# Kernel optimization log

Measured on AMD Instinct MI355X. Metric: run time of the kernel, lower is better.

Reference implementation:

```python
import jax, jax.numpy as jnp
import numpy as np

C = 512
GROUPS = 32
EPS = 1e-6


def setup_inputs() -> dict:
    key = jax.random.key(0)
    ks = jax.random.split(key, 10)
    B, H, W = 4, 64, 64
    s = 0.02
    return {
        "x": jax.random.normal(ks[0], (B, C, H, W), dtype=jnp.float32),
        "gamma": jnp.ones((C,), jnp.float32),
        "beta": jnp.zeros((C,), jnp.float32),
        "Wq": jax.random.normal(ks[1], (C, C), jnp.float32) * s,
        "bq": jnp.zeros((C,), jnp.float32),
        "Wk": jax.random.normal(ks[2], (C, C), jnp.float32) * s,
        "bk": jnp.zeros((C,), jnp.float32),
        "Wv": jax.random.normal(ks[3], (C, C), jnp.float32) * s,
        "bv": jnp.zeros((C,), jnp.float32),
        "Wo": jax.random.normal(ks[4], (C, C), jnp.float32) * s,
        "bo": jnp.zeros((C,), jnp.float32),
    }


def _group_norm(x, gamma, beta):
    B, Cc, H, W = x.shape
    xg = x.reshape(B, GROUPS, Cc // GROUPS, H, W)
    mean = jnp.mean(xg, axis=(2, 3, 4), keepdims=True)
    var = jnp.var(xg, axis=(2, 3, 4), keepdims=True)
    xn = ((xg - mean) * jax.lax.rsqrt(var + EPS)).reshape(B, Cc, H, W)
    return xn * gamma[None, :, None, None] + beta[None, :, None, None]


def _conv1x1(x, Wm, b):
    # x: [B,C,H,W], Wm: [Cout,Cin]
    return jnp.einsum('bchw,oc->bohw', x, Wm) + b[None, :, None, None]


def reference(x, gamma, beta, Wq, bq, Wk, bk, Wv, bv, Wo, bo):
    B, Cc, H, W = x.shape
    h = _group_norm(x, gamma, beta)
    q = _conv1x1(h, Wq, bq).reshape(B, Cc, H * W)  # [B,C,N]
    k = _conv1x1(h, Wk, bk).reshape(B, Cc, H * W)
    v = _conv1x1(h, Wv, bv).reshape(B, Cc, H * W)
    scale = float(Cc) ** (-0.5)
    # attn[b,i,j] = sum_c q[b,c,i] k[b,c,j]
    attn = jnp.einsum('bci,bcj->bij', q, k) * scale
    attn = jax.nn.softmax(attn, axis=2)
    # out[b,c,i] = sum_j v[b,c,j] attn[b,i,j]
    out = jnp.einsum('bcj,bij->bci', v, attn).reshape(B, Cc, H, W)
    out = _conv1x1(out, Wo, bo)
    return x + out
```

## Files before the change

kernel.cpp:

```cpp
#include <hip/hip_runtime.h>
#include <hip/hip_bf16.h>


#define C_DIM 512
#define N_SPA 4096
#define BATCH 4
#define NALL 16384

#define BM 128
#define BN 128
#define BK 32

typedef short short8 __attribute__((ext_vector_type(8)));
typedef short short4v __attribute__((ext_vector_type(4)));
typedef float float4v __attribute__((ext_vector_type(4)));

__device__ __forceinline__ short f2b(float f) {
  __hip_bfloat16 h = __float2bfloat16(f);
  return *reinterpret_cast<short*>(&h);
}
__device__ __forceinline__ float b2f(short s) {
  __hip_bfloat16 h;
  *reinterpret_cast<short*>(&h) = s;
  return __bfloat162float(h);
}

typedef __attribute__((address_space(1))) const void gvoid_t;
typedef __attribute__((address_space(3))) void lvoid_t;
__device__ __forceinline__ void gload16(const void* g, void* l) {
  __builtin_amdgcn_global_load_lds((gvoid_t*)g, (lvoid_t*)l, 16, 0, 0);
}

__global__ void wconv_kernel(const float* __restrict__ Wq, const float* __restrict__ Wk,
                             const float* __restrict__ Wv, const float* __restrict__ Wo,
                             const float* __restrict__ bq, const float* __restrict__ bk,
                             const float* __restrict__ bv,
                             short* __restrict__ out, float* __restrict__ bias_all) {
  int i = blockIdx.x * 256 + threadIdx.x;
  out[0 * 262144 + i] = f2b(Wq[i]);
  out[1 * 262144 + i] = f2b(Wk[i]);
  out[2 * 262144 + i] = f2b(Wv[i]);
  out[3 * 262144 + i] = f2b(Wo[i]);
  if (i < 1536) bias_all[i] = (i < 512) ? bq[i] : (i < 1024) ? bk[i - 512] : bv[i - 1024];
}

__global__ void gn_part(const float* __restrict__ x, float2* __restrict__ partials) {
  int grp = blockIdx.x >> 5, split = blockIdx.x & 31;
  const float4* xg = (const float4*)(x + (size_t)grp * 65536 + split * 2048);
  int t = threadIdx.x;
  float4 a = xg[t], b4 = xg[256 + t];
  float s = a.x + a.y + a.z + a.w + b4.x + b4.y + b4.z + b4.w;
  float ss = a.x * a.x + a.y * a.y + a.z * a.z + a.w * a.w +
             b4.x * b4.x + b4.y * b4.y + b4.z * b4.z + b4.w * b4.w;
  __shared__ float red[512];
  red[t] = s; red[256 + t] = ss;
  __syncthreads();
  for (int off = 128; off > 0; off >>= 1) {
    if (t < off) { red[t] += red[t + off]; red[256 + t] += red[256 + t + off]; }
    __syncthreads();
  }
  if (t == 0) partials[blockIdx.x] = make_float2(red[0], red[256]);
}

__global__ void gn_norm(const float* __restrict__ x, const float* __restrict__ gamma,
                        const float* __restrict__ beta, const float2* __restrict__ partials,
                        short* __restrict__ h_t) {
  int bid = blockIdx.x;
  int grp = bid >> 4, seg = bid & 15;
  int b = grp >> 5, g = grp & 31;
  float s = 0.f, ss = 0.f;
  for (int j = 0; j < 32; ++j) { float2 p2 = partials[grp * 32 + j]; s += p2.x; ss += p2.y; }
  float mean = s * (1.0f / 65536.0f);
  float rstd = rsqrtf(ss * (1.0f / 65536.0f) - mean * mean + 1e-6f);

  const float* xg = x + (size_t)grp * 65536 + seg * 256;
  __shared__ float tile[16][257];
  int t = threadIdx.x;
#pragma unroll
  for (int i = 0; i < 16; ++i) tile[i][t] = xg[(size_t)i * N_SPA + t];
  __syncthreads();

  int c8 = (t & 1) * 8, ci = g * 16 + c8;
  float ga[8], be[8];
#pragma unroll
  for (int j = 0; j < 8; ++j) { ga[j] = gamma[ci + j]; be[j] = beta[ci + j]; }
#pragma unroll
  for (int pass = 0; pass < 2; ++pass) {
    int nl = (t >> 1) + pass * 128;
    short8 o;
#pragma unroll
    for (int j = 0; j < 8; ++j) {
      float v = (tile[c8 + j][nl] - mean) * rstd * ga[j] + be[j];
      o[j] = f2b(v);
    }
    *(short8*)&h_t[((size_t)b * N_SPA + seg * 256 + nl) * C_DIM + ci] = o;
  }
}

template <int EPI>
__global__ __launch_bounds__(256) void gemm_bt(
    const short* __restrict__ A, const short* __restrict__ BT, void* __restrict__ Cout,
    const float* __restrict__ bias, const float* __restrict__ resid,
    int M, int N, int K, int lda, int ldb, int ldc,
    size_t az, size_t bz, size_t cz, float scale) {
  __shared__ __align__(16) short lds_a[BM * BK];
  __shared__ __align__(16) short lds_b[BN * BK];
  int t = threadIdx.x;
  int m0 = blockIdx.y * BM;
  int n0 = blockIdx.x * BN;
  int z = blockIdx.z;
  A += (size_t)z * az;
  BT += (size_t)z * bz;
  int w = t >> 6, l = t & 63;
  int wm = (w >> 1) * 64, wn = (w & 1) * 64;
  int lr = l & 15, lk = l >> 4;

  int sr = l >> 2, scol = (l & 3) * 8;
  const short* ga0 = A + (size_t)(m0 + w * 16 + sr) * lda + scol;
  const short* ga1 = ga0 + (size_t)64 * lda;
  const short* gb0 = BT + (size_t)(n0 + w * 16 + sr) * ldb + scol;
  const short* gb1 = gb0 + (size_t)64 * ldb;
  short* la0 = &lds_a[w * 16 * BK];
  short* la1 = &lds_a[(64 + w * 16) * BK];
  short* lb0 = &lds_b[w * 16 * BK];
  short* lb1 = &lds_b[(64 + w * 16) * BK];

  float4v acc[4][4];
#pragma unroll
  for (int i = 0; i < 4; ++i)
#pragma unroll
    for (int j = 0; j < 4; ++j) acc[i][j] = (float4v){0.f, 0.f, 0.f, 0.f};

  for (int k0 = 0; k0 < K; k0 += BK) {
    __syncthreads();
    gload16(ga0, la0); gload16(ga1, la1);
    gload16(gb0, lb0); gload16(gb1, lb1);
    ga0 += BK; ga1 += BK; gb0 += BK; gb1 += BK;
    __syncthreads();
    short8 af[4], bf[4];
#pragma unroll
    for (int i = 0; i < 4; ++i) af[i] = *(const short8*)&lds_a[(wm + i * 16 + lr) * BK + lk * 8];
#pragma unroll
    for (int i = 0; i < 4; ++i) bf[i] = *(const short8*)&lds_b[(wn + i * 16 + lr) * BK + lk * 8];
#pragma unroll
    for (int i = 0; i < 4; ++i)
#pragma unroll
      for (int j = 0; j < 4; ++j)
        acc[i][j] = __builtin_amdgcn_mfma_f32_16x16x32_bf16(af[i], bf[j], acc[i][j], 0, 0, 0);
  }

#pragma unroll
  for (int i = 0; i < 4; ++i)
#pragma unroll
    for (int j = 0; j < 4; ++j) {
      int mB = m0 + wm + i * 16 + lk * 4;
      int nn = n0 + wn + j * 16 + lr;
      if constexpr (EPI == 2) {
        short* outp = (short*)Cout + (size_t)z * cz;
#pragma unroll
        for (int r = 0; r < 4; ++r)
          outp[(size_t)(mB + r) * ldc + nn] = f2b(__expf(acc[i][j][r] * scale));
      } else if constexpr (EPI == 3) {
        short* outp = (short*)Cout + (size_t)z * cz;
        float inv = bias[(size_t)z * N_SPA + nn];
        short4v v;
#pragma unroll
        for (int r = 0; r < 4; ++r) v[r] = f2b(acc[i][j][r] * inv);
        *(short4v*)(outp + (size_t)nn * ldc + mB) = v;
      } else if constexpr (EPI == 4) {
        int bb = nn >> 12, n = nn & 4095;
        size_t base = ((size_t)bb * C_DIM + mB) * N_SPA + n;
#pragma unroll
        for (int r = 0; r < 4; ++r) {
          float f = acc[i][j][r] + bias[mB + r] + resid[base + (size_t)r * N_SPA];
          ((float*)Cout)[base + (size_t)r * N_SPA] = f;
        }
      } else {
        short* outp = (short*)Cout + (size_t)z * NALL * C_DIM;
        const float* bz_ = bias + (size_t)z * C_DIM;
        if (z < 2) {
          short4v v;
#pragma unroll
          for (int r = 0; r < 4; ++r) v[r] = f2b(acc[i][j][r] + bz_[mB + r]);
          *(short4v*)(outp + (size_t)nn * C_DIM + mB) = v;
        } else {
#pragma unroll
          for (int r = 0; r < 4; ++r)
            outp[(size_t)(mB + r) * NALL + nn] = f2b(acc[i][j][r] + bz_[mB + r]);
        }
      }
    }
}

__global__ void rowsum_kernel(const short* __restrict__ p, float* __restrict__ inv_sum) {
  size_t row = blockIdx.x;
  const short8* pr = (const short8*)(p + row * N_SPA);
  int t = threadIdx.x;
  short8 a = pr[t * 2], b = pr[t * 2 + 1];
  float s = 0.f;
#pragma unroll
  for (int j = 0; j < 8; ++j) s += b2f(a[j]) + b2f(b[j]);
  __shared__ float red[256];
  red[t] = s; __syncthreads();
  for (int off = 128; off > 0; off >>= 1) {
    if (t < off) red[t] += red[t + off];
    __syncthreads();
  }
  if (t == 0) inv_sum[row] = 1.0f / red[0];
}

extern "C" void kernel_launch(void* const* d_in, const int* in_sizes, int n_in,
                              void* d_out, int out_size, void* d_ws, size_t ws_size,
                              hipStream_t stream) {
  const float* x     = (const float*)d_in[0];
  const float* gamma = (const float*)d_in[1];
  const float* beta  = (const float*)d_in[2];
  const float* Wq = (const float*)d_in[3];  const float* bq = (const float*)d_in[4];
  const float* Wk = (const float*)d_in[5];  const float* bk = (const float*)d_in[6];
  const float* Wv = (const float*)d_in[7];  const float* bv = (const float*)d_in[8];
  const float* Wo = (const float*)d_in[9];  const float* bo = (const float*)d_in[10];
  float* out = (float*)d_out;

  short* Wb  = (short*)d_ws;
  short* h_t = Wb + 4 * 262144;
  short* q_t = h_t + (size_t)NALL * C_DIM;
  short* k_t = q_t + (size_t)NALL * C_DIM;
  short* v_  = k_t + (size_t)NALL * C_DIM;
  short* p   = v_  + (size_t)NALL * C_DIM;
  float* inv_sum = (float*)(p + (size_t)BATCH * N_SPA * N_SPA);
  float2* partials = (float2*)(inv_sum + NALL);
  float* bias_all = (float*)(partials + 4096);
  short* o_t = h_t;

  wconv_kernel<<<1024, 256, 0, stream>>>(Wq, Wk, Wv, Wo, bq, bk, bv, Wb, bias_all);
  gn_part<<<BATCH * 32 * 32, 256, 0, stream>>>(x, partials);
  gn_norm<<<BATCH * 32 * 16, 256, 0, stream>>>(x, gamma, beta, partials, h_t);

  const float scale = 0.04419417382415922f;
  const size_t pz = (size_t)N_SPA * N_SPA;
  const size_t hz = (size_t)N_SPA * C_DIM;

  gemm_bt<6><<<dim3(NALL / BN, C_DIM / BM, 3), 256, 0, stream>>>(
      Wb, h_t, q_t, bias_all, nullptr,
      C_DIM, NALL, C_DIM, C_DIM, C_DIM, C_DIM, 262144, 0, 0, 0.f);

  gemm_bt<2><<<dim3(N_SPA / BN, N_SPA / BM, BATCH), 256, 0, stream>>>(
      q_t, k_t, p, nullptr, nullptr,
      N_SPA, N_SPA, C_DIM, C_DIM, C_DIM, N_SPA, hz, hz, pz, scale);

  rowsum_kernel<<<NALL, 256, 0, stream>>>(p, inv_sum);

  gemm_bt<3><<<dim3(N_SPA / BN, C_DIM / BM, BATCH), 256, 0, stream>>>(
      v_, p, o_t, inv_sum, nullptr,
      C_DIM, N_SPA, N_SPA, NALL, N_SPA, C_DIM, N_SPA, pz, hz, 0.f);

  gemm_bt<4><<<dim3(NALL / BN, C_DIM / BM, 1), 256, 0, stream>>>(
      Wb + 3 * 262144, o_t, out, bo, x,
      C_DIM, NALL, C_DIM, C_DIM, C_DIM, 0, 0, 0, 0, 0.f);
}
```

Before: 405.1 us.

## Fuse softmax row sums into QK^T epilogue and deepen K tile for PV GEMM

```diff
diff --git a/kernel.cpp b/kernel.cpp
--- a/kernel.cpp
+++ b/kernel.cpp
@@ -9,7 +9,6 @@
 
 #define BM 128
 #define BN 128
-#define BK 32
 
 typedef short short8 __attribute__((ext_vector_type(8)));
 typedef short short4v __attribute__((ext_vector_type(4)));
@@ -97,14 +96,18 @@
   }
 }
 
-template <int EPI>
+template <int EPI, int BKT = 32>
 __global__ __launch_bounds__(256) void gemm_bt(
     const short* __restrict__ A, const short* __restrict__ BT, void* __restrict__ Cout,
-    const float* __restrict__ bias, const float* __restrict__ resid,
+    const float* __restrict__ bias, const float* __restrict__ resid, float* __restrict__ sums,
     int M, int N, int K, int lda, int ldb, int ldc,
     size_t az, size_t bz, size_t cz, float scale) {
-  __shared__ __align__(16) short lds_a[BM * BK];
-  __shared__ __align__(16) short lds_b[BN * BK];
+  __shared__ __align__(16) short lds_a[BM * BKT];
+  __shared__ __align__(16) short lds_b[BN * BKT];
+  constexpr int ROWS_PER = 2048 / BKT;
+  constexpr int ROUNDS = BM / ROWS_PER;
+  constexpr int RPW = ROWS_PER / 4;
+
   int t = threadIdx.x;
   int m0 = blockIdx.y * BM;
   int n0 = blockIdx.x * BN;
@@ -115,15 +118,18 @@
   int wm = (w >> 1) * 64, wn = (w & 1) * 64;
   int lr = l & 15, lk = l >> 4;
 
-  int sr = l >> 2, scol = (l & 3) * 8;
-  const short* ga0 = A + (size_t)(m0 + w * 16 + sr) * lda + scol;
-  const short* ga1 = ga0 + (size_t)64 * lda;
-  const short* gb0 = BT + (size_t)(n0 + w * 16 + sr) * ldb + scol;
-  const short* gb1 = gb0 + (size_t)64 * ldb;
-  short* la0 = &lds_a[w * 16 * BK];
-  short* la1 = &lds_a[(64 + w * 16) * BK];
-  short* lb0 = &lds_b[w * 16 * BK];
-  short* lb1 = &lds_b[(64 + w * 16) * BK];
+  int srow = l / (BKT / 8);
+  int scol = (l % (BKT / 8)) * 8;
+  const short* ga[ROUNDS]; const short* gb[ROUNDS];
+  short* la[ROUNDS]; short* lb[ROUNDS];
+#pragma unroll
+  for (int rr = 0; rr < ROUNDS; ++rr) {
+    int rbase = rr * ROWS_PER + w * RPW;
+    ga[rr] = A + (size_t)(m0 + rbase + srow) * lda + scol;
+    gb[rr] = BT + (size_t)(n0 + rbase + srow) * ldb + scol;
+    la[rr] = &lds_a[rbase * BKT];
+    lb[rr] = &lds_b[rbase * BKT];
+  }
 
   float4v acc[4][4];
 #pragma unroll
@@ -131,22 +137,37 @@
 #pragma unroll
     for (int j = 0; j < 4; ++j) acc[i][j] = (float4v){0.f, 0.f, 0.f, 0.f};
 
-  for (int k0 = 0; k0 < K; k0 += BK) {
+  for (int k0 = 0; k0 < K; k0 += BKT) {
     __syncthreads();
-    gload16(ga0, la0); gload16(ga1, la1);
-    gload16(gb0, lb0); gload16(gb1, lb1);
-    ga0 += BK; ga1 += BK; gb0 += BK; gb1 += BK;
+#pragma unroll
+    for (int rr = 0; rr < ROUNDS; ++rr) {
+      gload16(ga[rr], la[rr]); gload16(gb[rr], lb[rr]);
+      ga[rr] += BKT; gb[rr] += BKT;
+    }
     __syncthreads();
-    short8 af[4], bf[4];
-#pragma unroll
-    for (int i = 0; i < 4; ++i) af[i] = *(const short8*)&lds_a[(wm + i * 16 + lr) * BK + lk * 8];
-#pragma unroll
-    for (int i = 0; i < 4; ++i) bf[i] = *(const short8*)&lds_b[(wn + i * 16 + lr) * BK + lk * 8];
+#pragma unroll
+    for (int kk = 0; kk < BKT / 32; ++kk) {
+      short8 af[4], bf[4];
+#pragma unroll
+      for (int i = 0; i < 4; ++i)
+        af[i] = *(const short8*)&lds_a[(wm + i * 16 + lr) * BKT + kk * 32 + lk * 8];
+#pragma unroll
+      for (int i = 0; i < 4; ++i)
+        bf[i] = *(const short8*)&lds_b[(wn + i * 16 + lr) * BKT + kk * 32 + lk * 8];
+#pragma unroll
+      for (int i = 0; i < 4; ++i)
+#pragma unroll
+        for (int j = 0; j < 4; ++j)
+          acc[i][j] = __builtin_amdgcn_mfma_f32_16x16x32_bf16(af[i], bf[j], acc[i][j], 0, 0, 0);
+    }
+  }
+
+  float rowsum[4][4];
+  if constexpr (EPI == 2) {
 #pragma unroll
     for (int i = 0; i < 4; ++i)
 #pragma unroll
-      for (int j = 0; j < 4; ++j)
-        acc[i][j] = __builtin_amdgcn_mfma_f32_16x16x32_bf16(af[i], bf[j], acc[i][j], 0, 0, 0);
+      for (int r = 0; r < 4; ++r) rowsum[i][r] = 0.f;
   }
 
 #pragma unroll
@@ -158,11 +179,14 @@
       if constexpr (EPI == 2) {
         short* outp = (short*)Cout + (size_t)z * cz;
 #pragma unroll
-        for (int r = 0; r < 4; ++r)
-          outp[(size_t)(mB + r) * ldc + nn] = f2b(__expf(acc[i][j][r] * scale));
+        for (int r = 0; r < 4; ++r) {
+          float e = __expf(acc[i][j][r] * scale);
+          rowsum[i][r] += e;
+          outp[(size_t)(mB + r) * ldc + nn] = f2b(e);
+        }
       } else if constexpr (EPI == 3) {
         short* outp = (short*)Cout + (size_t)z * cz;
-        float inv = bias[(size_t)z * N_SPA + nn];
+        float inv = 1.0f / sums[(size_t)z * N_SPA + nn];
         short4v v;
 #pragma unroll
         for (int r = 0; r < 4; ++r) v[r] = f2b(acc[i][j][r] * inv);
@@ -190,23 +214,19 @@
         }
       }
     }
-}
-
-__global__ void rowsum_kernel(const short* __restrict__ p, float* __restrict__ inv_sum) {
-  size_t row = blockIdx.x;
-  const short8* pr = (const short8*)(p + row * N_SPA);
-  int t = threadIdx.x;
-  short8 a = pr[t * 2], b = pr[t * 2 + 1];
-  float s = 0.f;
-#pragma unroll
-  for (int j = 0; j < 8; ++j) s += b2f(a[j]) + b2f(b[j]);
-  __shared__ float red[256];
-  red[t] = s; __syncthreads();
-  for (int off = 128; off > 0; off >>= 1) {
-    if (t < off) red[t] += red[t + off];
-    __syncthreads();
-  }
-  if (t == 0) inv_sum[row] = 1.0f / red[0];
+
+  if constexpr (EPI == 2) {
+#pragma unroll
+    for (int i = 0; i < 4; ++i)
+#pragma unroll
+      for (int r = 0; r < 4; ++r) {
+        float s = rowsum[i][r];
+        s += __shfl_xor(s, 1); s += __shfl_xor(s, 2);
+        s += __shfl_xor(s, 4); s += __shfl_xor(s, 8);
+        if (lr == 0)
+          atomicAdd(&sums[(size_t)z * N_SPA + m0 + wm + i * 16 + lk * 4 + r], s);
+      }
+  }
 }
 
 extern "C" void kernel_launch(void* const* d_in, const int* in_sizes, int n_in,
@@ -227,34 +247,33 @@
   short* k_t = q_t + (size_t)NALL * C_DIM;
   short* v_  = k_t + (size_t)NALL * C_DIM;
   short* p   = v_  + (size_t)NALL * C_DIM;
-  float* inv_sum = (float*)(p + (size_t)BATCH * N_SPA * N_SPA);
-  float2* partials = (float2*)(inv_sum + NALL);
+  float* sums = (float*)(p + (size_t)BATCH * N_SPA * N_SPA);
+  float2* partials = (float2*)(sums + NALL);
   float* bias_all = (float*)(partials + 4096);
   short* o_t = h_t;
 
   wconv_kernel<<<1024, 256, 0, stream>>>(Wq, Wk, Wv, Wo, bq, bk, bv, Wb, bias_all);
   gn_part<<<BATCH * 32 * 32, 256, 0, stream>>>(x, partials);
   gn_norm<<<BATCH * 32 * 16, 256, 0, stream>>>(x, gamma, beta, partials, h_t);
+  hipMemsetAsync(sums, 0, NALL * sizeof(float), stream);
 
   const float scale = 0.04419417382415922f;
   const size_t pz = (size_t)N_SPA * N_SPA;
   const size_t hz = (size_t)N_SPA * C_DIM;
 
   gemm_bt<6><<<dim3(NALL / BN, C_DIM / BM, 3), 256, 0, stream>>>(
-      Wb, h_t, q_t, bias_all, nullptr,
+      Wb, h_t, q_t, bias_all, nullptr, nullptr,
       C_DIM, NALL, C_DIM, C_DIM, C_DIM, C_DIM, 262144, 0, 0, 0.f);
 
   gemm_bt<2><<<dim3(N_SPA / BN, N_SPA / BM, BATCH), 256, 0, stream>>>(
-      q_t, k_t, p, nullptr, nullptr,
+      q_t, k_t, p, nullptr, nullptr, sums,
       N_SPA, N_SPA, C_DIM, C_DIM, C_DIM, N_SPA, hz, hz, pz, scale);
 
-  rowsum_kernel<<<NALL, 256, 0, stream>>>(p, inv_sum);
-
-  gemm_bt<3><<<dim3(N_SPA / BN, C_DIM / BM, BATCH), 256, 0, stream>>>(
-      v_, p, o_t, inv_sum, nullptr,
+  gemm_bt<3, 64><<<dim3(N_SPA / BN, C_DIM / BM, BATCH), 256, 0, stream>>>(
+      v_, p, o_t, nullptr, nullptr, sums,
       C_DIM, N_SPA, N_SPA, NALL, N_SPA, C_DIM, N_SPA, pz, hz, 0.f);
 
   gemm_bt<4><<<dim3(NALL / BN, C_DIM / BM, 1), 256, 0, stream>>>(
-      Wb + 3 * 262144, o_t, out, bo, x,
+      Wb + 3 * 262144, o_t, out, bo, x, nullptr,
       C_DIM, NALL, C_DIM, C_DIM, C_DIM, 0, 0, 0, 0, 0.f);
 }
```

Result: no change. 398.0 us (-1.8%).
